# Kernel optimization log

Measured on AMD Instinct MI355X. Metric: run time of the kernel, lower is better.

## Reference

```python
import jax, jax.numpy as jnp
import numpy as np

WS = 8          # window size
NH = 12         # num heads
DEPTH = 2       # blocks: W-MSA, SW-MSA
EPS = 1e-6
N = WS * WS     # tokens per window


def _rel_index():
    c = np.stack(np.meshgrid(np.arange(WS), np.arange(WS), indexing='ij')).reshape(2, -1)
    rel = (c[:, :, None] - c[:, None, :]).transpose(1, 2, 0)
    rel[:, :, 0] += WS - 1
    rel[:, :, 1] += WS - 1
    rel[:, :, 0] *= 2 * WS - 1
    return rel.sum(-1)  # [N, N] int

REL_IDX = jnp.asarray(_rel_index())


def _shift_mask(H, W, shift):
    # static (numpy) construction, H/W/shift are Python ints
    img = np.zeros((H, W))
    cnt = 0
    for hs in (slice(0, -WS), slice(-WS, -shift), slice(-shift, None)):
        for wsl in (slice(0, -WS), slice(-WS, -shift), slice(-shift, None)):
            img[hs, wsl] = cnt
            cnt += 1
    win = img.reshape(H // WS, WS, W // WS, WS).transpose(0, 2, 1, 3).reshape(-1, N)
    diff = win[:, None, :] - win[:, :, None]
    return jnp.asarray(np.where(diff != 0, -100.0, 0.0), jnp.float32)  # [nW, N, N]


def _ln(x):
    m = x.mean(-1, keepdims=True)
    v = ((x - m) ** 2).mean(-1, keepdims=True)
    return (x - m) * jax.lax.rsqrt(v + EPS)


def _block(x, H, W, emb, p, shift):
    qkv_w, qkv_b, proj_w, proj_b, ff1_w, ff1_b, ff2_w, ff2_b, ada_w, ada_b, bias_table = p
    B, L, C = x.shape
    hd = C // NH
    ada = jax.nn.silu(emb) @ ada_w.T + ada_b  # [B, 6C]
    sh_sa, sc_sa, g_sa, sh_ff, sc_ff, g_ff = jnp.split(ada, 6, axis=-1)
    h = _ln(x) * (1.0 + sc_sa[:, None]) + sh_sa[:, None]
    h = h.reshape(B, H, W, C)
    if shift > 0:
        h = jnp.roll(h, (-shift, -shift), (1, 2))
    # window partition -> [B*nW, N, C]
    win = h.reshape(B, H // WS, WS, W // WS, WS, C).transpose(0, 1, 3, 2, 4, 5).reshape(-1, N, C)
    B_ = win.shape[0]
    qkv = (win @ qkv_w.T + qkv_b).reshape(B_, N, 3, NH, hd)
    q, k, v = qkv[:, :, 0], qkv[:, :, 1], qkv[:, :, 2]
    attn = jnp.einsum('bnhd,bmhd->bhnm', q, k) * (hd ** -0.5)
    bias = bias_table[REL_IDX]  # [N, N, NH]
    attn = attn + bias.transpose(2, 0, 1)[None]
    if shift > 0:
        mask = _shift_mask(H, W, shift)  # [nW, N, N]
        nW = mask.shape[0]
        attn = (attn.reshape(B, nW, NH, N, N) + mask[None, :, None]).reshape(B_, NH, N, N)
    attn = jax.nn.softmax(attn, axis=-1)
    out = jnp.einsum('bhnm,bmhd->bnhd', attn, v).reshape(B_, N, C)
    out = out @ proj_w.T + proj_b
    # window reverse
    h = out.reshape(B, H // WS, W // WS, WS, WS, C).transpose(0, 1, 3, 2, 4, 5).reshape(B, H, W, C)
    if shift > 0:
        h = jnp.roll(h, (shift, shift), (1, 2))
    x = x + g_sa[:, None] * h.reshape(B, L, C)
    h2 = _ln(x) * (1.0 + sc_ff[:, None]) + sh_ff[:, None]
    ff = jax.nn.gelu(h2 @ ff1_w.T + ff1_b, approximate=False) @ ff2_w.T + ff2_b
    return x + g_ff[:, None] * ff


def _forward(x, emb, H, W, params):
    for i in range(DEPTH):
        p = tuple(a[i] for a in params)
        x = _block(x, H, W, emb, p, 0 if i % 2 == 0 else WS // 2)
    return x


def setup_inputs() -> dict:
    key = jax.random.key(0)
    ks = jax.random.split(key, 16)
    C, E, FF = 384, 384, 4 * 384
    B, H, W = 8, 64, 64
    p = lambda k, shape: jax.random.normal(k, shape, jnp.float32) * 0.02
    return {
        'x': jax.random.normal(ks[0], (B, H * W, C), jnp.float32),
        'H': H,
        'W': W,
        'emb': jax.random.normal(ks[1], (B, E), jnp.float32),
        'qkv_w': p(ks[2], (DEPTH, 3 * C, C)),
        'qkv_b': p(ks[3], (DEPTH, 3 * C)),
        'proj_w': p(ks[4], (DEPTH, C, C)),
        'proj_b': p(ks[5], (DEPTH, C)),
        'ff1_w': p(ks[6], (DEPTH, FF, C)),
        'ff1_b': p(ks[7], (DEPTH, FF)),
        'ff2_w': p(ks[8], (DEPTH, C, FF)),
        'ff2_b': p(ks[9], (DEPTH, C)),
        'ada_w': p(ks[10], (DEPTH, 6 * C, E)),
        'ada_b': p(ks[11], (DEPTH, 6 * C)),
        'bias_table': p(ks[12], (DEPTH, (2 * WS - 1) ** 2, NH)),
    }


def reference(x, H, W, emb, qkv_w, qkv_b, proj_w, proj_b, ff1_w, ff1_b, ff2_w, ff2_b, ada_w, ada_b, bias_table):
    params = (qkv_w, qkv_b, proj_w, proj_b, ff1_w, ff1_b, ff2_w, ff2_b, ada_w, ada_b, bias_table)
    return _forward(x, emb, H, W, params)
```

## Files before the change

### kernel.cpp

```cpp
#include <hip/hip_runtime.h>

typedef __bf16 bf16_t;
typedef bf16_t bf16x8 __attribute__((ext_vector_type(8)));
typedef float f32x4 __attribute__((ext_vector_type(4)));

#define EPI_STORE 0
#define EPI_GELU 1
#define EPI_RES_WIN 2
#define EPI_RES_ID 3

__device__ __forceinline__ float bf2f(unsigned short u) {
    union { unsigned int i; float f; } x; x.i = ((unsigned int)u) << 16; return x.f;
}
__device__ __forceinline__ unsigned short f2bf(float f) {
    union { __bf16 h; unsigned short u; } c; c.h = (__bf16)f; return c.u;
}
__device__ __forceinline__ float gelu_f(float v) {
    float u = v * (0.7978845608f + 0.0356774081f * v * v);
    return v / (1.0f + __expf(-2.0f * u));
}

__device__ __forceinline__ void async_cp16(const unsigned short* g, unsigned short* l) {
    __builtin_amdgcn_global_load_lds(
        (const __attribute__((address_space(1))) unsigned int*)g,
        (__attribute__((address_space(3))) unsigned int*)l, 16, 0, 0);
}

__device__ __forceinline__ int map_win(int m, int shift) {
    int n = m & 63, w = m >> 6;
    int b = w >> 6, ww = w & 63;
    int hh = ((ww >> 3) * 8 + (n >> 3) + shift) & 63;
    int wc = ((ww & 7) * 8 + (n & 7) + shift) & 63;
    return (b << 12) + (hh << 6) + wc;
}


__global__ void f2bf4_kernel(const float* __restrict__ s0, const float* __restrict__ s1,
                             const float* __restrict__ s2, const float* __restrict__ s3,
                             unsigned short* __restrict__ dst) {
    int i = blockIdx.x * 256 + threadIdx.x;
    const float* s; int off;
    if (i < 884736)       { s = s0; off = 0; }
    else if (i < 1179648) { s = s1; off = 884736; }
    else if (i < 2359296) { s = s2; off = 1179648; }
    else                  { s = s3; off = 2359296; }
    dst[i] = f2bf(s[i - off]);
}

__global__ void silu_kernel(const float* __restrict__ emb,
                            float* __restrict__ out, int n) {
    int i = blockIdx.x * 256 + threadIdx.x;
    if (i < n) { float e = emb[i]; out[i] = e / (1.0f + expf(-e)); }
}

__global__ __launch_bounds__(64) void ada_kernel(
    const float* __restrict__ se,
    const float* __restrict__ ada_w,
    const float* __restrict__ ada_b,
    float* __restrict__ ada_out)
{
    int j = blockIdx.x;
    int layer = blockIdx.y;
    int t = threadIdx.x;
    const float* wr = ada_w + ((long)layer * 2304 + j) * 384;
    float w[6];
#pragma unroll
    for (int q = 0; q < 6; q++) w[q] = wr[t + 64 * q];
    float bias = ada_b[layer * 2304 + j];
    for (int b = 0; b < 8; b++) {
        float p = 0.f;
#pragma unroll
        for (int q = 0; q < 6; q++) p += se[b * 384 + t + 64 * q] * w[q];
#pragma unroll
        for (int o = 32; o > 0; o >>= 1) p += __shfl_xor(p, o);
        if (t == 0) ada_out[((long)layer * 8 + b) * 2304 + j] = p + bias;
    }
}

__global__ __launch_bounds__(256) void ln_mod_kernel(
    const float* __restrict__ x, const float* __restrict__ ada,
    unsigned short* __restrict__ h, int sh_off, int sc_off)
{
    int row = blockIdx.x * 4 + (threadIdx.x >> 6);
    int b = row >> 12;
    int t = threadIdx.x & 63;
    const float* xr = x + (long)row * 384;
    float v[6];
    float s = 0.f;
#pragma unroll
    for (int j = 0; j < 6; j++) { v[j] = xr[t + 64 * j]; s += v[j]; }
#pragma unroll
    for (int o = 32; o > 0; o >>= 1) s += __shfl_xor(s, o);
    float mean = s * (1.0f / 384.0f);
    float s2 = 0.f;
#pragma unroll
    for (int j = 0; j < 6; j++) { float d = v[j] - mean; s2 += d * d; }
#pragma unroll
    for (int o = 32; o > 0; o >>= 1) s2 += __shfl_xor(s2, o);
    float rstd = rsqrtf(s2 * (1.0f / 384.0f) + 1e-6f);
    const float* adab = ada + (long)b * 2304;
#pragma unroll
    for (int j = 0; j < 6; j++) {
        int c = t + 64 * j;
        float val = (v[j] - mean) * rstd * (1.0f + adab[sc_off + c]) + adab[sh_off + c];
        h[(long)row * 384 + c] = f2bf(val);
    }
}


template <int EPI, bool GATHER, bool RESINIT>
__global__ __launch_bounds__(256) void gemm128(
    const unsigned short* __restrict__ A,
    const unsigned short* __restrict__ W,
    const float* __restrict__ bias,
    unsigned short* __restrict__ out,
    float* __restrict__ xres,
    const float* __restrict__ xbase,
    const float* __restrict__ gvec,
    int M, int N, int K, int shift)
{
    __shared__ __align__(16) unsigned short Sh[17408];
    unsigned short* As = Sh;
    unsigned short* Bs = Sh + 8192;

    const int tid = threadIdx.x;
    const int wv = tid >> 6, lane = tid & 63;

    const int nx = gridDim.x, ny = gridDim.y;
    const int lin = blockIdx.y * nx + blockIdx.x;
    const int xcd = lin & 7, p = lin >> 3;
    const int m0 = (xcd * (ny >> 3) + p / nx) * 128;
    const int n0 = (p % nx) * 128;

    const int r8 = lane >> 3;
    const int cofs = ((lane & 7) ^ r8) * 8;
    long arow[4], brow[4];
#pragma unroll
    for (int t = 0; t < 4; t++) {
        int rl = wv * 32 + t * 8 + r8;
        arow[t] = GATHER ? (long)map_win(m0 + rl, shift) : (long)(m0 + rl);
        brow[t] = (long)(n0 + rl);
    }

    const int wm = (wv >> 1) * 64, wn = (wv & 1) * 64;
    const int l16 = lane & 15, quad = lane >> 4;
    const int swz = l16 & 7;

    f32x4 acc[4][4] = {};

    for (int k0 = 0; k0 < K; k0 += 64) {
#pragma unroll
        for (int t = 0; t < 4; t++) {
            async_cp16(A + arow[t] * K + k0 + cofs, As + (wv * 32 + t * 8) * 64);
            async_cp16(W + brow[t] * K + k0 + cofs, Bs + (wv * 32 + t * 8) * 64);
        }
        __syncthreads();

#pragma unroll
        for (int kk = 0; kk < 2; kk++) {
            bf16x8 af[4], bfr[4];
#pragma unroll
            for (int i = 0; i < 4; i++)
                af[i] = *(const bf16x8*)&As[(wm + i * 16 + l16) * 64 +
                                            (((kk * 4 + quad) ^ swz) * 8)];
#pragma unroll
            for (int j = 0; j < 4; j++)
                bfr[j] = *(const bf16x8*)&Bs[(wn + j * 16 + l16) * 64 +
                                             (((kk * 4 + quad) ^ swz) * 8)];
#pragma unroll
            for (int i = 0; i < 4; i++)
#pragma unroll
                for (int j = 0; j < 4; j++)
                    acc[i][j] = __builtin_amdgcn_mfma_f32_16x16x32_bf16(af[i], bfr[j], acc[i][j], 0, 0, 0);
        }
        __syncthreads();
    }

    float bv[4];
#pragma unroll
    for (int j = 0; j < 4; j++) bv[j] = bias[n0 + wn + j * 16 + l16];

    unsigned short* Cs = Sh;
#pragma unroll
    for (int i = 0; i < 4; i++)
#pragma unroll
        for (int j = 0; j < 4; j++)
#pragma unroll
            for (int r = 0; r < 4; r++) {
                float v = acc[i][j][r] + bv[j];
                if constexpr (EPI == EPI_GELU) v = gelu_f(v);
                Cs[(wm + i * 16 + quad * 4 + r) * 136 + wn + j * 16 + l16] = f2bf(v);
            }
    __syncthreads();

#pragma unroll
    for (int kseg = 0; kseg < 8; kseg++) {
        int s = tid + 256 * kseg;
        int row = s >> 4, c8 = (s & 15) << 3;
        bf16x8 val = *(const bf16x8*)&Cs[row * 136 + c8];
        if constexpr (EPI == EPI_STORE || EPI == EPI_GELU) {
            *(bf16x8*)&out[(long)(m0 + row) * N + n0 + c8] = val;
        } else {
            long dst = (EPI == EPI_RES_WIN) ? (long)map_win(m0 + row, shift)
                                            : (long)(m0 + row);
            float* xrow = xres + dst * 384 + n0 + c8;
            const float* grow = gvec + (long)(dst >> 12) * 2304 + n0 + c8;
#pragma unroll
            for (int e = 0; e < 8; e++) {
                float v = (float)val[e];
                float base;
                if constexpr (RESINIT) base = xbase[dst * 384 + n0 + c8 + e];
                else                   base = xrow[e];
                xrow[e] = base + grow[e] * v;
            }
        }
    }
}


__device__ __forceinline__ int reg3(int p) { return (p < 56) ? 0 : ((p < 60) ? 1 : 2); }

__global__ __launch_bounds__(256) void attn_kernel(
    const unsigned short* __restrict__ qkv,
    const float* __restrict__ bias_table,
    unsigned short* __restrict__ out,
    int shift)
{
    __shared__ unsigned short Pl[4][64 * 68];
    __shared__ unsigned short VTl[4][32 * 68];

    const int wv = threadIdx.x >> 6, lane = threadIdx.x & 63;
    const int head = blockIdx.x * 4 + wv;
    const int win = blockIdx.y;
    const int l16 = lane & 15, quad = lane >> 4;

    unsigned short* P = Pl[wv];
    unsigned short* vt = VTl[wv];

    const long base = (long)win * 64 * 1152 + head * 32;

    bf16x8 qf[4], kf[4];
#pragma unroll
    for (int i = 0; i < 4; i++) {
        qf[i] = *(const bf16x8*)&qkv[base + (long)(i * 16 + l16) * 1152 + quad * 8];
        kf[i] = *(const bf16x8*)&qkv[base + 384 + (long)(i * 16 + l16) * 1152 + quad * 8];
    }
    {
        const uint4* vp = (const uint4*)&qkv[base + 768 + (long)lane * 1152];
#pragma unroll
        for (int c4 = 0; c4 < 4; c4++) {
            uint4 v = vp[c4];
            unsigned int u[4] = {v.x, v.y, v.z, v.w};
#pragma unroll
            for (int e = 0; e < 4; e++) {
                vt[(c4 * 8 + e * 2) * 68 + lane]     = (unsigned short)(u[e] & 0xffffu);
                vt[(c4 * 8 + e * 2 + 1) * 68 + lane] = (unsigned short)(u[e] >> 16);
            }
        }
    }

    f32x4 sacc[4][4] = {};
#pragma unroll
    for (int i = 0; i < 4; i++)
#pragma unroll
        for (int j = 0; j < 4; j++)
            sacc[i][j] = __builtin_amdgcn_mfma_f32_16x16x32_bf16(qf[i], kf[j], sacc[i][j], 0, 0, 0);

    const float scale = 0.17677669529663687f;
    const int ww = win & 63, wi = ww >> 3, wj = ww & 7;

#pragma unroll
    for (int i = 0; i < 4; i++) {
#pragma unroll
        for (int r = 0; r < 4; r++) {
            int n = i * 16 + quad * 4 + r;
            int nr = n >> 3, nc = n & 7;
            int labq = (shift > 0) ? reg3(wi * 8 + nr) * 3 + reg3(wj * 8 + nc) : 0;
            float v[4];
#pragma unroll
            for (int j = 0; j < 4; j++) {
                int m = j * 16 + l16;
                int mr = m >> 3, mc = m & 7;
                float s = sacc[i][j][r] * scale +
                          bias_table[((nr - mr + 7) * 15 + (nc - mc + 7)) * 12 + head];
                if (shift > 0) {
                    int labm = reg3(wi * 8 + mr) * 3 + reg3(wj * 8 + mc);
                    if (labm != labq) s -= 100.0f;
                }
                v[j] = s;
            }
            float mx = fmaxf(fmaxf(v[0], v[1]), fmaxf(v[2], v[3]));
#pragma unroll
            for (int o = 1; o < 16; o <<= 1) mx = fmaxf(mx, __shfl_xor(mx, o));
            float sum = 0.f;
#pragma unroll
            for (int j = 0; j < 4; j++) { v[j] = __expf(v[j] - mx); sum += v[j]; }
#pragma unroll
            for (int o = 1; o < 16; o <<= 1) sum += __shfl_xor(sum, o);
            float inv = 1.0f / sum;
#pragma unroll
            for (int j = 0; j < 4; j++)
                P[n * 68 + j * 16 + l16] = f2bf(v[j] * inv);
        }
    }
    __syncthreads();

    f32x4 oacc[4][2] = {};
#pragma unroll
    for (int kt = 0; kt < 2; kt++) {
        bf16x8 pf[4], vf[2];
#pragma unroll
        for (int i = 0; i < 4; i++)
            pf[i] = *(const bf16x8*)&P[(i * 16 + l16) * 68 + kt * 32 + quad * 8];
#pragma unroll
        for (int jt = 0; jt < 2; jt++)
            vf[jt] = *(const bf16x8*)&vt[(jt * 16 + l16) * 68 + kt * 32 + quad * 8];
#pragma unroll
        for (int i = 0; i < 4; i++)
#pragma unroll
            for (int jt = 0; jt < 2; jt++)
                oacc[i][jt] = __builtin_amdgcn_mfma_f32_16x16x32_bf16(pf[i], vf[jt], oacc[i][jt], 0, 0, 0);
    }

#pragma unroll
    for (int i = 0; i < 4; i++)
#pragma unroll
        for (int jt = 0; jt < 2; jt++)
#pragma unroll
            for (int r = 0; r < 4; r++) {
                int row = i * 16 + quad * 4 + r;
                int col = jt * 16 + l16;
                out[((long)win * 64 + row) * 384 + head * 32 + col] = f2bf(oacc[i][jt][r]);
            }
}


extern "C" void kernel_launch(void* const* d_in, const int* in_sizes, int n_in,
                              void* d_out, int out_size, void* d_ws, size_t ws_size,
                              hipStream_t stream) {
    const float* x_in   = (const float*)d_in[0];
    const float* emb    = (const float*)d_in[3];
    const float* qkv_w  = (const float*)d_in[4];
    const float* qkv_b  = (const float*)d_in[5];
    const float* proj_w = (const float*)d_in[6];
    const float* proj_b = (const float*)d_in[7];
    const float* ff1_w  = (const float*)d_in[8];
    const float* ff1_b  = (const float*)d_in[9];
    const float* ff2_w  = (const float*)d_in[10];
    const float* ff2_b  = (const float*)d_in[11];
    const float* ada_w  = (const float*)d_in[12];
    const float* ada_b  = (const float*)d_in[13];
    const float* bias_t = (const float*)d_in[14];

    char* ws = (char*)d_ws;
    unsigned short* h_buf   = (unsigned short*)ws;
    unsigned short* big_buf = (unsigned short*)(ws + 25165824);
    unsigned short* wqkv    = (unsigned short*)(ws + 125829120);
    unsigned short* wproj   = (unsigned short*)(ws + 127598592);
    unsigned short* wff1    = (unsigned short*)(ws + 128188416);
    unsigned short* wff2    = (unsigned short*)(ws + 130547712);
    float*          ada_out = (float*)(ws + 132907008);
    float*          se      = (float*)(ws + 133054464);

    float* x_acc = (float*)d_out;

    const int M = 32768;

    f2bf4_kernel<<<13824, 256, 0, stream>>>(qkv_w, proj_w, ff1_w, ff2_w, wqkv);

    silu_kernel<<<(3072 + 255) / 256, 256, 0, stream>>>(emb, se, 3072);
    ada_kernel<<<dim3(2304, 2), 64, 0, stream>>>(se, ada_w, ada_b, ada_out);

    for (int layer = 0; layer < 2; layer++) {
        const int shift = layer ? 4 : 0;
        const float* ada_l = ada_out + (long)layer * 8 * 2304;

        ln_mod_kernel<<<M / 4, 256, 0, stream>>>(layer == 0 ? x_in : x_acc,
                                                 ada_l, h_buf, 0, 384);

        gemm128<EPI_STORE, true, false><<<dim3(9, 256), 256, 0, stream>>>(
            h_buf, wqkv + (long)layer * 1152 * 384, qkv_b + layer * 1152,
            big_buf, nullptr, nullptr, nullptr, M, 1152, 384, shift);

        attn_kernel<<<dim3(3, 512), 256, 0, stream>>>(
            big_buf, bias_t + layer * 225 * 12, h_buf, shift);

        if (layer == 0) {
            gemm128<EPI_RES_WIN, false, true><<<dim3(3, 256), 256, 0, stream>>>(
                h_buf, wproj, proj_b,
                nullptr, x_acc, x_in, ada_l + 768, M, 384, 384, shift);
        } else {
            gemm128<EPI_RES_WIN, false, false><<<dim3(3, 256), 256, 0, stream>>>(
                h_buf, wproj + (long)384 * 384, proj_b + 384,
                nullptr, x_acc, nullptr, ada_l + 768, M, 384, 384, shift);
        }

        ln_mod_kernel<<<M / 4, 256, 0, stream>>>(x_acc, ada_l, h_buf, 1152, 1536);

        gemm128<EPI_GELU, false, false><<<dim3(12, 256), 256, 0, stream>>>(
            h_buf, wff1 + (long)layer * 1536 * 384, ff1_b + layer * 1536,
            big_buf, nullptr, nullptr, nullptr, M, 1536, 384, 0);

        gemm128<EPI_RES_ID, false, false><<<dim3(3, 256), 256, 0, stream>>>(
            big_buf, wff2 + (long)layer * 384 * 1536, ff2_b + layer * 384,
            nullptr, x_acc, nullptr, ada_l + 1920, M, 384, 1536, 0);
    }
}
```

Baseline: 686.9 us.

## Double-buffer GEMM K-loop with BK=32 and write epilogue directly from registers

The GEMM main loop drops BK from 64 to 32 and uses two LDS buffers. The next tile's async global-to-LDS copy is now issued before the current tile's MFMAs, with one barrier per iteration, so loads overlap compute. The MFMA operands are swapped so each lane holds four consecutive output columns. This lets the epilogue write bias/GELU results and residual updates straight from registers as ushort4/float4, removing the LDS staging pass and a barrier. Launch bounds now request 4 blocks per CU, which can limit registers. The shorter K-step halves the MFMA work per barrier, and the epilogue stores are narrower and less coalesced than the previous 16-byte row-contiguous writes.

```diff
diff --git a/kernel.cpp b/kernel.cpp
--- a/kernel.cpp
+++ b/kernel.cpp
@@ -109,7 +109,7 @@
 
 
 template <int EPI, bool GATHER, bool RESINIT>
-__global__ __launch_bounds__(256) void gemm128(
+__global__ __launch_bounds__(256, 4) void gemm128(
     const unsigned short* __restrict__ A,
     const unsigned short* __restrict__ W,
     const float* __restrict__ bias,
@@ -119,7 +119,7 @@
     const float* __restrict__ gvec,
     int M, int N, int K, int shift)
 {
-    __shared__ __align__(16) unsigned short Sh[17408];
+    __shared__ __align__(16) unsigned short Sh[16384];
     unsigned short* As = Sh;
     unsigned short* Bs = Sh + 8192;
 
@@ -132,86 +132,96 @@
     const int m0 = (xcd * (ny >> 3) + p / nx) * 128;
     const int n0 = (p % nx) * 128;
 
-    const int r8 = lane >> 3;
-    const int cofs = ((lane & 7) ^ r8) * 8;
-    long arow[4], brow[4];
-#pragma unroll
-    for (int t = 0; t < 4; t++) {
-        int rl = wv * 32 + t * 8 + r8;
+    const int r4 = lane >> 2;
+    const int cofs = ((lane & 3) ^ (r4 & 3)) * 8;
+    long arow[2], brow[2];
+#pragma unroll
+    for (int t = 0; t < 2; t++) {
+        int rl = wv * 32 + t * 16 + r4;
         arow[t] = GATHER ? (long)map_win(m0 + rl, shift) : (long)(m0 + rl);
         brow[t] = (long)(n0 + rl);
     }
 
     const int wm = (wv >> 1) * 64, wn = (wv & 1) * 64;
     const int l16 = lane & 15, quad = lane >> 4;
-    const int swz = l16 & 7;
+    const int rswz = (quad ^ (l16 & 3)) * 8;
 
     f32x4 acc[4][4] = {};
-
-    for (int k0 = 0; k0 < K; k0 += 64) {
-#pragma unroll
-        for (int t = 0; t < 4; t++) {
-            async_cp16(A + arow[t] * K + k0 + cofs, As + (wv * 32 + t * 8) * 64);
-            async_cp16(W + brow[t] * K + k0 + cofs, Bs + (wv * 32 + t * 8) * 64);
+    const int niter = K >> 5;
+
+#pragma unroll
+    for (int t = 0; t < 2; t++) {
+        async_cp16(A + arow[t] * K + cofs, As + (wv * 32 + t * 16) * 32);
+        async_cp16(W + brow[t] * K + cofs, Bs + (wv * 32 + t * 16) * 32);
+    }
+
+    for (int it = 0; it < niter; it++) {
+        __syncthreads();
+        if (it + 1 < niter) {
+            int k0 = (it + 1) << 5;
+            int b = (it + 1) & 1;
+#pragma unroll
+            for (int t = 0; t < 2; t++) {
+                async_cp16(A + arow[t] * K + k0 + cofs, As + b * 4096 + (wv * 32 + t * 16) * 32);
+                async_cp16(W + brow[t] * K + k0 + cofs, Bs + b * 4096 + (wv * 32 + t * 16) * 32);
+            }
         }
-        __syncthreads();
-
-#pragma unroll
-        for (int kk = 0; kk < 2; kk++) {
-            bf16x8 af[4], bfr[4];
-#pragma unroll
-            for (int i = 0; i < 4; i++)
-                af[i] = *(const bf16x8*)&As[(wm + i * 16 + l16) * 64 +
-                                            (((kk * 4 + quad) ^ swz) * 8)];
+        const unsigned short* Ac = As + (it & 1) * 4096;
+        const unsigned short* Bc = Bs + (it & 1) * 4096;
+        bf16x8 af[4], bfr[4];
+#pragma unroll
+        for (int i = 0; i < 4; i++)
+            af[i] = *(const bf16x8*)&Ac[(wm + i * 16 + l16) * 32 + rswz];
+#pragma unroll
+        for (int j = 0; j < 4; j++)
+            bfr[j] = *(const bf16x8*)&Bc[(wn + j * 16 + l16) * 32 + rswz];
+#pragma unroll
+        for (int i = 0; i < 4; i++)
 #pragma unroll
             for (int j = 0; j < 4; j++)
-                bfr[j] = *(const bf16x8*)&Bs[(wn + j * 16 + l16) * 64 +
-                                             (((kk * 4 + quad) ^ swz) * 8)];
-#pragma unroll
-            for (int i = 0; i < 4; i++)
-#pragma unroll
-                for (int j = 0; j < 4; j++)
-                    acc[i][j] = __builtin_amdgcn_mfma_f32_16x16x32_bf16(af[i], bfr[j], acc[i][j], 0, 0, 0);
-        }
-        __syncthreads();
-    }
-
-    float bv[4];
-#pragma unroll
-    for (int j = 0; j < 4; j++) bv[j] = bias[n0 + wn + j * 16 + l16];
-
-    unsigned short* Cs = Sh;
-#pragma unroll
-    for (int i = 0; i < 4; i++)
-#pragma unroll
-        for (int j = 0; j < 4; j++)
-#pragma unroll
-            for (int r = 0; r < 4; r++) {
-                float v = acc[i][j][r] + bv[j];
-                if constexpr (EPI == EPI_GELU) v = gelu_f(v);
-                Cs[(wm + i * 16 + quad * 4 + r) * 136 + wn + j * 16 + l16] = f2bf(v);
-            }
-    __syncthreads();
-
-#pragma unroll
-    for (int kseg = 0; kseg < 8; kseg++) {
-        int s = tid + 256 * kseg;
-        int row = s >> 4, c8 = (s & 15) << 3;
-        bf16x8 val = *(const bf16x8*)&Cs[row * 136 + c8];
+                acc[i][j] = __builtin_amdgcn_mfma_f32_16x16x32_bf16(bfr[j], af[i], acc[i][j], 0, 0, 0);
+    }
+
+    float4 bv4[4];
+#pragma unroll
+    for (int j = 0; j < 4; j++)
+        bv4[j] = *(const float4*)&bias[n0 + wn + j * 16 + quad * 4];
+
+#pragma unroll
+    for (int i = 0; i < 4; i++) {
+        int row = m0 + wm + i * 16 + l16;
         if constexpr (EPI == EPI_STORE || EPI == EPI_GELU) {
-            *(bf16x8*)&out[(long)(m0 + row) * N + n0 + c8] = val;
+            unsigned short* orow = out + (long)row * N + n0 + wn + quad * 4;
+#pragma unroll
+            for (int j = 0; j < 4; j++) {
+                float v0 = acc[i][j][0] + bv4[j].x;
+                float v1 = acc[i][j][1] + bv4[j].y;
+                float v2 = acc[i][j][2] + bv4[j].z;
+                float v3 = acc[i][j][3] + bv4[j].w;
+                if constexpr (EPI == EPI_GELU) {
+                    v0 = gelu_f(v0); v1 = gelu_f(v1); v2 = gelu_f(v2); v3 = gelu_f(v3);
+                }
+                ushort4 pk = { f2bf(v0), f2bf(v1), f2bf(v2), f2bf(v3) };
+                *(ushort4*)&orow[j * 16] = pk;
+            }
         } else {
-            long dst = (EPI == EPI_RES_WIN) ? (long)map_win(m0 + row, shift)
-                                            : (long)(m0 + row);
-            float* xrow = xres + dst * 384 + n0 + c8;
-            const float* grow = gvec + (long)(dst >> 12) * 2304 + n0 + c8;
-#pragma unroll
-            for (int e = 0; e < 8; e++) {
-                float v = (float)val[e];
-                float base;
-                if constexpr (RESINIT) base = xbase[dst * 384 + n0 + c8 + e];
-                else                   base = xrow[e];
-                xrow[e] = base + grow[e] * v;
+            long dst = (EPI == EPI_RES_WIN) ? (long)map_win(row, shift) : (long)row;
+            float* xrow = xres + dst * 384 + n0 + wn + quad * 4;
+            const float* grow = gvec + (long)(dst >> 12) * 2304 + n0 + wn + quad * 4;
+#pragma unroll
+            for (int j = 0; j < 4; j++) {
+                float4 gv = *(const float4*)&grow[j * 16];
+                float4 xb;
+                if constexpr (RESINIT)
+                    xb = *(const float4*)&xbase[dst * 384 + n0 + wn + quad * 4 + j * 16];
+                else
+                    xb = *(const float4*)&xrow[j * 16];
+                float4 o;
+                o.x = xb.x + gv.x * (acc[i][j][0] + bv4[j].x);
+                o.y = xb.y + gv.y * (acc[i][j][1] + bv4[j].y);
+                o.z = xb.z + gv.z * (acc[i][j][2] + bv4[j].z);
+                o.w = xb.w + gv.w * (acc[i][j][3] + bv4[j].w);
+                *(float4*)&xrow[j * 16] = o;
             }
         }
     }
```

Result: slower. 712.4 us (+3.7%).
